# Performance work log

Measured on AMD Instinct MI355X. Metric: run time of the kernel, lower is better.

The kernel has to match this reference:

```python
import jax, jax.numpy as jnp
import numpy as np

B, T, D, H = 2, 2048, 2048, 16
HD = D // H  # head_dim = 128


def setup_inputs() -> dict:
    key = jax.random.key(0)
    ks = jax.random.split(key, 7)
    s = 1.0 / np.sqrt(D)
    return {
        "x": jax.random.normal(ks[0], (B, T, D), jnp.float32),
        "Wq": jax.random.normal(ks[1], (D, D), jnp.float32) * s,
        "Wk": jax.random.normal(ks[2], (D, D), jnp.float32) * s,
        "Wv": jax.random.normal(ks[3], (D, D), jnp.float32) * s,
        "Wo": jax.random.normal(ks[4], (D, D), jnp.float32) * s,
        "rope_cos": jax.random.uniform(ks[5], (T, HD), jnp.float32, -1.0, 1.0),
        "rope_sin": jax.random.uniform(ks[6], (T, HD), jnp.float32, -1.0, 1.0),
    }


def _rope(x, cos, sin):
    # x: [B,H,T,HD]; cos/sin: [T,HD] broadcast over batch/heads
    half = x.shape[-1] // 2
    lhs, rhs = x[..., :half], x[..., half:]
    rotated = jnp.concatenate((-rhs, lhs), axis=-1)
    return cos[None, None] * x + rotated * sin[None, None]


def reference(x, Wq, Wk, Wv, Wo, rope_cos, rope_sin):
    Bc, Tc, Dc = x.shape
    # torch nn.Linear: y = x @ W.T
    q = (x @ Wq.T).reshape(Bc, Tc, H, HD).transpose(0, 2, 1, 3)
    k = (x @ Wk.T).reshape(Bc, Tc, H, HD).transpose(0, 2, 1, 3)
    v = (x @ Wv.T).reshape(Bc, Tc, H, HD).transpose(0, 2, 1, 3)
    q = _rope(q, rope_cos[:Tc], rope_sin[:Tc])
    k = _rope(k, rope_cos[:Tc], rope_sin[:Tc])
    scores = jnp.einsum('bhqd,bhkd->bhqk', q, k) / jnp.sqrt(jnp.float32(HD))
    causal = jnp.triu(jnp.ones((Tc, Tc), bool), k=1)
    scores = jnp.where(causal[None, None], -jnp.inf, scores)
    attn = jax.nn.softmax(scores, axis=-1)
    ctx = jnp.einsum('bhqk,bhkd->bhqd', attn, v)
    ctx = ctx.transpose(0, 2, 1, 3).reshape(Bc, Tc, Dc)
    return ctx @ Wo.T
```

## Files before the change

kernel.cpp:

```cpp
#include <hip/hip_runtime.h>

typedef __attribute__((ext_vector_type(4))) float   f32x4;
typedef __attribute__((ext_vector_type(8))) __bf16  bf16x8;
typedef __attribute__((ext_vector_type(4))) __bf16  bf16x4;
typedef __attribute__((ext_vector_type(8))) unsigned short u16x8;

#define NH   16
#define HD   128
#define TSEQ 2048
#define DM   2048
#define MT   4096

__device__ __forceinline__ f32x4 mfma_bf16(bf16x8 a, bf16x8 b, f32x4 c) {
  return __builtin_amdgcn_mfma_f32_16x16x32_bf16(a, b, c, 0, 0, 0);
}

__device__ __forceinline__ void gl_lds16(const __bf16* g, __bf16* l) {
  __builtin_amdgcn_global_load_lds(
      (const __attribute__((address_space(1))) void*)g,
      (__attribute__((address_space(3))) void*)l, 16, 0, 0);
}

__global__ __launch_bounds__(256) void k_cvtw(
    const float* __restrict__ X,
    const float* __restrict__ W0, const float* __restrict__ W1,
    const float* __restrict__ W2, const float* __restrict__ W3,
    __bf16* __restrict__ DX,
    __bf16* __restrict__ D0, __bf16* __restrict__ D1,
    __bf16* __restrict__ D2, __bf16* __restrict__ D3) {
  int z = blockIdx.z;
  const float* s = (z == 0) ? W0 : (z == 1) ? W1 : (z == 2) ? W2
                   : (z == 3) ? W3 : X;
  __bf16*      d = (z == 0) ? D0 : (z == 1) ? D1 : (z == 2) ? D2
                   : (z == 3) ? D3 : DX;
  int n4 = (z == 4) ? (MT * DM / 4) : (DM * DM / 4);
  int i = blockIdx.x * 256 + threadIdx.x;
  int stride = gridDim.x * 256;
  for (; i < n4; i += stride) {
    f32x4 v = ((const f32x4*)s)[i];
    bf16x4 o;
    o[0] = (__bf16)v[0]; o[1] = (__bf16)v[1];
    o[2] = (__bf16)v[2]; o[3] = (__bf16)v[3];
    ((bf16x4*)d)[i] = o;
  }
}

template <int MODE>
__global__ __launch_bounds__(256) void k_gemm(const __bf16* __restrict__ A,
                                              const __bf16* __restrict__ Bm,
                                              __bf16* __restrict__ Dst,
                                              float* __restrict__ F) {
  __shared__ __bf16 As[128 * 32];
  __shared__ __bf16 Bs[128 * 32];

  const int bid = blockIdx.x;
  const int wg  = (bid & 7) * 64 + (bid >> 3);
  const int n0  = (wg & 15) * 128;
  const int m0  = (wg >> 4) * 128;

  const int tid  = threadIdx.x;
  const int lane = tid & 63, w = tid >> 6;
  const int g    = lane >> 4, li = lane & 15;
  const int wr   = w >> 1, wc = w & 1;
  const int srow = lane >> 2;
  const int sseg = lane & 3;

  const f32x4 zero = {0.f, 0.f, 0.f, 0.f};
  f32x4 acc[4][4];
#pragma unroll
  for (int i = 0; i < 4; i++)
#pragma unroll
    for (int j = 0; j < 4; j++) acc[i][j] = zero;

  for (int k0 = 0; k0 < DM; k0 += 32) {
#pragma unroll
    for (int c = 0; c < 2; c++) {
      const int ch = w * 2 + c;
      gl_lds16(&A[(size_t)(m0 + ch * 16 + srow) * DM + k0 + sseg * 8],
               &As[ch * 512]);
      gl_lds16(&Bm[(size_t)(n0 + ch * 16 + srow) * DM + k0 + sseg * 8],
               &Bs[ch * 512]);
    }
    __syncthreads();
    bf16x8 af[4], bfr[4];
#pragma unroll
    for (int i = 0; i < 4; i++)
      af[i] = *(const bf16x8*)&As[(wr * 64 + i * 16 + li) * 32 + g * 8];
#pragma unroll
    for (int i = 0; i < 4; i++)
      bfr[i] = *(const bf16x8*)&Bs[(wc * 64 + i * 16 + li) * 32 + g * 8];
#pragma unroll
    for (int mi = 0; mi < 4; mi++)
#pragma unroll
      for (int ni = 0; ni < 4; ni++)
        acc[mi][ni] = mfma_bf16(af[mi], bfr[ni], acc[mi][ni]);
    __syncthreads();
  }

#pragma unroll
  for (int mi = 0; mi < 4; mi++)
#pragma unroll
    for (int ni = 0; ni < 4; ni++) {
      int colb = n0 + wc * 64 + ni * 16 + li;
#pragma unroll
      for (int r = 0; r < 4; r++) {
        int rowb = m0 + wr * 64 + mi * 16 + g * 4 + r;
        float vv = acc[mi][ni][r];
        if (MODE == 0) {
          F[(size_t)rowb * DM + colb] = vv;
        } else {
          int h = colb >> 7, d = colb & 127;
          int b = rowb >> 11, t = rowb & 2047;
          Dst[(((size_t)(b * NH + h)) * TSEQ + t) * HD + d] = (__bf16)vv;
        }
      }
    }
}

__global__ __launch_bounds__(256) void k_rope(__bf16* __restrict__ q,
                                              __bf16* __restrict__ kk,
                                              const float* __restrict__ rc,
                                              const float* __restrict__ rs) {
  int gid    = blockIdx.x * 256 + threadIdx.x;
  int tensor = gid >> 20;
  int rem    = gid & ((1 << 20) - 1);
  int bh     = rem >> 15;
  int r2     = rem & 32767;
  int t      = r2 >> 4;
  int j      = r2 & 15;
  int d0     = j * 4;
  __bf16* base = (tensor ? kk : q) + ((size_t)bh * TSEQ + t) * HD;
  f32x4 ca = *(const f32x4*)&rc[t * HD + d0];
  f32x4 cb = *(const f32x4*)&rc[t * HD + d0 + 64];
  f32x4 sa = *(const f32x4*)&rs[t * HD + d0];
  f32x4 sb = *(const f32x4*)&rs[t * HD + d0 + 64];
  bf16x4 xa = *(bf16x4*)&base[d0];
  bf16x4 xb = *(bf16x4*)&base[d0 + 64];
  bf16x4 oa, ob;
#pragma unroll
  for (int u = 0; u < 4; u++) {
    float fa = (float)xa[u], fb = (float)xb[u];
    oa[u] = (__bf16)(ca[u] * fa - fb * sa[u]);
    ob[u] = (__bf16)(cb[u] * fb + fa * sb[u]);
  }
  *(bf16x4*)&base[d0]      = oa;
  *(bf16x4*)&base[d0 + 64] = ob;
}

__global__ __launch_bounds__(256) void k_trans(const __bf16* __restrict__ v,
                                               __bf16* __restrict__ vt) {
  __shared__ unsigned short tile[64][73];
  int bh = blockIdx.z;
  int t0 = blockIdx.x * 64, d0 = blockIdx.y * 64;
  int tid = threadIdx.x;
  int r = tid >> 2, s4 = tid & 3;
  const unsigned short* src =
      (const unsigned short*)v + ((size_t)bh * TSEQ + t0) * HD + d0;
  u16x8 a = *(const u16x8*)&src[(size_t)r * HD + s4 * 16];
  u16x8 b = *(const u16x8*)&src[(size_t)r * HD + s4 * 16 + 8];
#pragma unroll
  for (int u = 0; u < 8; u++) {
    tile[r][s4 * 16 + u]     = a[u];
    tile[r][s4 * 16 + 8 + u] = b[u];
  }
  __syncthreads();
  unsigned short* dst =
      (unsigned short*)vt + ((size_t)bh * HD + d0) * TSEQ + t0;
  u16x8 o1, o2;
#pragma unroll
  for (int u = 0; u < 8; u++) {
    o1[u] = tile[s4 * 16 + u][r];
    o2[u] = tile[s4 * 16 + 8 + u][r];
  }
  *(u16x8*)&dst[(size_t)r * TSEQ + s4 * 16]     = o1;
  *(u16x8*)&dst[(size_t)r * TSEQ + s4 * 16 + 8] = o2;
}

__global__ __launch_bounds__(256, 2) void k_attn(const __bf16* __restrict__ q,
                                                 const __bf16* __restrict__ k,
                                                 const __bf16* __restrict__ vt,
                                                 __bf16* __restrict__ ctx) {
  __shared__ __bf16 Ks[64 * 136];
  __shared__ __bf16 Vs[128 * 72];
  __shared__ __bf16 Ps[4][32 * 72];

  const int bid = blockIdx.x;
  const int wg  = (bid & 7) * 64 + (bid >> 3);
  const int bh  = wg >> 4;
  const int qt  = 15 - (wg & 15);
  const int q0  = qt * 128;

  const int tid  = threadIdx.x;
  const int lane = tid & 63, w = tid >> 6;
  const int g    = lane >> 4, li = lane & 15;
  const int qw   = q0 + w * 32;

  const __bf16* qb = q  + (size_t)bh * TSEQ * HD;
  const __bf16* kb = k  + (size_t)bh * TSEQ * HD;
  const __bf16* vb = vt + (size_t)bh * HD * TSEQ;

  const float CST = 0.08838834764831845f * 1.4426950408889634f;
  bf16x8 qf[2][4];
#pragma unroll
  for (int s = 0; s < 2; s++)
#pragma unroll
    for (int kc = 0; kc < 4; kc++) {
      bf16x8 t =
          *(const bf16x8*)&qb[(size_t)(qw + s * 16 + li) * HD + kc * 32 + g * 8];
      bf16x8 o;
#pragma unroll
      for (int e = 0; e < 8; e++) o[e] = (__bf16)((float)t[e] * CST);
      qf[s][kc] = o;
    }

  const f32x4 zero = {0.f, 0.f, 0.f, 0.f};
  f32x4 o[2][8];
#pragma unroll
  for (int s = 0; s < 2; s++)
#pragma unroll
    for (int dt = 0; dt < 8; dt++) o[s][dt] = zero;
  float mrow[2][4], lrow[2][4];
#pragma unroll
  for (int s = 0; s < 2; s++)
#pragma unroll
    for (int r = 0; r < 4; r++) { mrow[s][r] = -1e30f; lrow[s][r] = 0.f; }

  const int nkt = 2 * qt + 2;

  const int kR = tid >> 4, kS = tid & 15;
  const int vR = tid >> 3, vS = tid & 7;

  bf16x8 pk[4], pv[4];
#pragma unroll
  for (int i = 0; i < 4; i++) {
    pk[i] = *(const bf16x8*)&kb[(size_t)(kR + 16 * i) * HD + kS * 8];
    pv[i] = *(const bf16x8*)&vb[(size_t)(vR + 32 * i) * TSEQ + vS * 8];
  }

  for (int kt = 0; kt < nkt; kt++) {
    const int kv0 = kt * 64;
    __syncthreads();
#pragma unroll
    for (int i = 0; i < 4; i++)
      *(bf16x8*)&Ks[(kR + 16 * i) * 136 + kS * 8] = pk[i];
#pragma unroll
    for (int i = 0; i < 4; i++)
      *(bf16x8*)&Vs[(vR + 32 * i) * 72 + vS * 8] = pv[i];
    if (kt + 1 < nkt) {
      const int nv0 = kv0 + 64;
#pragma unroll
      for (int i = 0; i < 4; i++) {
        pk[i] = *(const bf16x8*)&kb[(size_t)(nv0 + kR + 16 * i) * HD + kS * 8];
        pv[i] = *(const bf16x8*)&vb[(size_t)(vR + 32 * i) * TSEQ + nv0 + vS * 8];
      }
    }
    __syncthreads();

    if (kv0 <= qw + 31) {
      f32x4 sc[2][4];
#pragma unroll
      for (int s = 0; s < 2; s++)
#pragma unroll
        for (int kvf = 0; kvf < 4; kvf++) sc[s][kvf] = zero;
#pragma unroll
      for (int kvf = 0; kvf < 4; kvf++)
#pragma unroll
        for (int kc = 0; kc < 4; kc++) {
          bf16x8 kf =
              *(const bf16x8*)&Ks[(kvf * 16 + li) * 136 + kc * 32 + g * 8];
          sc[0][kvf] = mfma_bf16(qf[0][kc], kf, sc[0][kvf]);
          sc[1][kvf] = mfma_bf16(qf[1][kc], kf, sc[1][kvf]);
        }
      if (kv0 + 63 > qw) {
#pragma unroll
        for (int s = 0; s < 2; s++)
#pragma unroll
          for (int kvf = 0; kvf < 4; kvf++) {
            int kg = kv0 + kvf * 16 + li;
#pragma unroll
            for (int r = 0; r < 4; r++) {
              int qg = qw + s * 16 + g * 4 + r;
              if (kg > qg) sc[s][kvf][r] = -1e30f;
            }
          }
      }
      float mnew[2][4];
      bool upd = false;
#pragma unroll
      for (int s = 0; s < 2; s++)
#pragma unroll
        for (int r = 0; r < 4; r++) {
          float a = fmaxf(fmaxf(sc[s][0][r], sc[s][1][r]),
                          fmaxf(sc[s][2][r], sc[s][3][r]));
          a = fmaxf(a, __shfl_xor(a, 1));
          a = fmaxf(a, __shfl_xor(a, 2));
          a = fmaxf(a, __shfl_xor(a, 4));
          a = fmaxf(a, __shfl_xor(a, 8));
          mnew[s][r] = fmaxf(mrow[s][r], a);
          upd = upd || (a > mrow[s][r]);
        }
      if (__any(upd)) {
#pragma unroll
        for (int s = 0; s < 2; s++)
#pragma unroll
          for (int r = 0; r < 4; r++) {
            float fac = __builtin_amdgcn_exp2f(mrow[s][r] - mnew[s][r]);
            mrow[s][r] = mnew[s][r];
            lrow[s][r] *= fac;
#pragma unroll
            for (int dt = 0; dt < 8; dt++) o[s][dt][r] *= fac;
          }
      }
#pragma unroll
      for (int s = 0; s < 2; s++)
#pragma unroll
        for (int kvf = 0; kvf < 4; kvf++) {
#pragma unroll
          for (int r = 0; r < 4; r++) {
            float p = __builtin_amdgcn_exp2f(sc[s][kvf][r] - mrow[s][r]);
            lrow[s][r] += p;
            Ps[w][(s * 16 + g * 4 + r) * 72 + kvf * 16 + li] = (__bf16)p;
          }
        }
      bf16x8 pa[2][2];
#pragma unroll
      for (int s = 0; s < 2; s++)
#pragma unroll
        for (int kvs = 0; kvs < 2; kvs++)
          pa[s][kvs] =
              *(const bf16x8*)&Ps[w][(s * 16 + li) * 72 + kvs * 32 + g * 8];
#pragma unroll
      for (int dt = 0; dt < 8; dt++) {
        bf16x8 v0 = *(const bf16x8*)&Vs[(dt * 16 + li) * 72 + g * 8];
        bf16x8 v1 = *(const bf16x8*)&Vs[(dt * 16 + li) * 72 + 32 + g * 8];
        o[0][dt] = mfma_bf16(pa[0][0], v0, o[0][dt]);
        o[0][dt] = mfma_bf16(pa[0][1], v1, o[0][dt]);
        o[1][dt] = mfma_bf16(pa[1][0], v0, o[1][dt]);
        o[1][dt] = mfma_bf16(pa[1][1], v1, o[1][dt]);
      }
    }
  }

  const int b = bh >> 4, h = bh & 15;
#pragma unroll
  for (int s = 0; s < 2; s++)
#pragma unroll
    for (int r = 0; r < 4; r++) {
      float l = lrow[s][r];
      l += __shfl_xor(l, 1);
      l += __shfl_xor(l, 2);
      l += __shfl_xor(l, 4);
      l += __shfl_xor(l, 8);
      float inv = 1.0f / l;
      size_t rowoff =
          ((size_t)(b * TSEQ + qw + s * 16 + g * 4 + r)) * DM + h * HD;
#pragma unroll
      for (int dt = 0; dt < 8; dt++)
        ctx[rowoff + dt * 16 + li] = (__bf16)(o[s][dt][r] * inv);
    }
}

extern "C" void kernel_launch(void* const* d_in, const int* in_sizes, int n_in,
                              void* d_out, int out_size, void* d_ws,
                              size_t ws_size, hipStream_t stream) {
  const float* x  = (const float*)d_in[0];
  const float* Wq = (const float*)d_in[1];
  const float* Wk = (const float*)d_in[2];
  const float* Wv = (const float*)d_in[3];
  const float* Wo = (const float*)d_in[4];
  const float* rc = (const float*)d_in[5];
  const float* rs = (const float*)d_in[6];
  float* out = (float*)d_out;

  __bf16* xb   = (__bf16*)d_ws;
  __bf16* wqb  = xb  + (size_t)MT * DM;
  __bf16* wkb  = wqb + (size_t)DM * DM;
  __bf16* wvb  = wkb + (size_t)DM * DM;
  __bf16* wob  = wvb + (size_t)DM * DM;
  __bf16* qbuf = wob + (size_t)DM * DM;
  __bf16* kbuf = qbuf + (size_t)MT * DM;
  __bf16* vbuf = kbuf + (size_t)MT * DM;
  __bf16* vtb  = vbuf + (size_t)MT * DM;
  __bf16* ctxb = vbuf;

  dim3 gw(1024, 1, 5);
  k_cvtw<<<gw, 256, 0, stream>>>(x, Wq, Wk, Wv, Wo, xb, wqb, wkb, wvb, wob);

  k_gemm<1><<<512, 256, 0, stream>>>(xb, wqb, qbuf, nullptr);
  k_gemm<1><<<512, 256, 0, stream>>>(xb, wkb, kbuf, nullptr);
  k_gemm<1><<<512, 256, 0, stream>>>(xb, wvb, vbuf, nullptr);

  k_rope<<<8192, 256, 0, stream>>>(qbuf, kbuf, rc, rs);

  dim3 gt(TSEQ / 64, HD / 64, 32);
  k_trans<<<gt, 256, 0, stream>>>(vbuf, vtb);

  k_attn<<<512, 256, 0, stream>>>(qbuf, kbuf, vtb, ctxb);

  k_gemm<0><<<512, 256, 0, stream>>>(ctxb, wob, nullptr, out);
}
```

Baseline: 456.9 us.

## Transpose QK^T MFMA so each lane owns one query row in softmax

Swaps the MFMA operand order for the score computation so the accumulator layout puts one query row per lane, with the KV positions spread over the four register elements. Row max and row sum then reduce mostly within a thread, needing 2 cross-lane shuffles instead of 4 per row, and per-thread softmax state shrinks from 8 to 2 scalars. P is written to LDS as packed 4-element vectors rather than scalar bf16 stores. In exchange, rescale factors and final inverses must be broadcast back to the O accumulator layout with extra __shfl calls, which adds cross-lane traffic on rescale steps.

Result: faster. 435.7 us (-4.6%).

```diff
diff --git a/kernel.cpp b/kernel.cpp
--- a/kernel.cpp
+++ b/kernel.cpp
@@ -219,11 +219,8 @@
   for (int s = 0; s < 2; s++)
 #pragma unroll
     for (int dt = 0; dt < 8; dt++) o[s][dt] = zero;
-  float mrow[2][4], lrow[2][4];
-#pragma unroll
-  for (int s = 0; s < 2; s++)
-#pragma unroll
-    for (int r = 0; r < 4; r++) { mrow[s][r] = -1e30f; lrow[s][r] = 0.f; }
+  float mrow[2] = {-1e30f, -1e30f};
+  float lrow[2] = {0.f, 0.f};
 
   const int nkt = 2 * qt + 2;
 
@@ -268,60 +265,68 @@
         for (int kc = 0; kc < 4; kc++) {
           bf16x8 kf =
               *(const bf16x8*)&Ks[(kvf * 16 + li) * 136 + kc * 32 + g * 8];
-          sc[0][kvf] = mfma_bf16(qf[0][kc], kf, sc[0][kvf]);
-          sc[1][kvf] = mfma_bf16(qf[1][kc], kf, sc[1][kvf]);
+          sc[0][kvf] = mfma_bf16(kf, qf[0][kc], sc[0][kvf]);
+          sc[1][kvf] = mfma_bf16(kf, qf[1][kc], sc[1][kvf]);
         }
       if (kv0 + 63 > qw) {
 #pragma unroll
-        for (int s = 0; s < 2; s++)
+        for (int s = 0; s < 2; s++) {
+          const int qg = qw + s * 16 + li;
 #pragma unroll
           for (int kvf = 0; kvf < 4; kvf++) {
-            int kg = kv0 + kvf * 16 + li;
 #pragma unroll
             for (int r = 0; r < 4; r++) {
-              int qg = qw + s * 16 + g * 4 + r;
+              int kg = kv0 + kvf * 16 + g * 4 + r;
               if (kg > qg) sc[s][kvf][r] = -1e30f;
             }
           }
-      }
-      float mnew[2][4];
+        }
+      }
+      float mnew[2];
       bool upd = false;
 #pragma unroll
-      for (int s = 0; s < 2; s++)
-#pragma unroll
-        for (int r = 0; r < 4; r++) {
-          float a = fmaxf(fmaxf(sc[s][0][r], sc[s][1][r]),
-                          fmaxf(sc[s][2][r], sc[s][3][r]));
-          a = fmaxf(a, __shfl_xor(a, 1));
-          a = fmaxf(a, __shfl_xor(a, 2));
-          a = fmaxf(a, __shfl_xor(a, 4));
-          a = fmaxf(a, __shfl_xor(a, 8));
-          mnew[s][r] = fmaxf(mrow[s][r], a);
-          upd = upd || (a > mrow[s][r]);
-        }
+      for (int s = 0; s < 2; s++) {
+        float a = fmaxf(fmaxf(sc[s][0][0], sc[s][0][1]),
+                        fmaxf(sc[s][0][2], sc[s][0][3]));
+#pragma unroll
+        for (int kvf = 1; kvf < 4; kvf++) {
+          float b0 = fmaxf(sc[s][kvf][0], sc[s][kvf][1]);
+          float b1 = fmaxf(sc[s][kvf][2], sc[s][kvf][3]);
+          a = fmaxf(a, fmaxf(b0, b1));
+        }
+        a = fmaxf(a, __shfl_xor(a, 16));
+        a = fmaxf(a, __shfl_xor(a, 32));
+        mnew[s] = fmaxf(mrow[s], a);
+        upd = upd || (a > mrow[s]);
+      }
       if (__any(upd)) {
 #pragma unroll
-        for (int s = 0; s < 2; s++)
+        for (int s = 0; s < 2; s++) {
+          float fc = __builtin_amdgcn_exp2f(mrow[s] - mnew[s]);
+          mrow[s] = mnew[s];
+          lrow[s] *= fc;
 #pragma unroll
           for (int r = 0; r < 4; r++) {
-            float fac = __builtin_amdgcn_exp2f(mrow[s][r] - mnew[s][r]);
-            mrow[s][r] = mnew[s][r];
-            lrow[s][r] *= fac;
-#pragma unroll
-            for (int dt = 0; dt < 8; dt++) o[s][dt][r] *= fac;
+            float fr = __shfl(fc, (lane & 48) | (g * 4 + r));
+#pragma unroll
+            for (int dt = 0; dt < 8; dt++) o[s][dt][r] *= fr;
           }
-      }
-#pragma unroll
-      for (int s = 0; s < 2; s++)
+        }
+      }
+#pragma unroll
+      for (int s = 0; s < 2; s++) {
 #pragma unroll
         for (int kvf = 0; kvf < 4; kvf++) {
+          bf16x4 pk4;
 #pragma unroll
           for (int r = 0; r < 4; r++) {
-            float p = __builtin_amdgcn_exp2f(sc[s][kvf][r] - mrow[s][r]);
-            lrow[s][r] += p;
-            Ps[w][(s * 16 + g * 4 + r) * 72 + kvf * 16 + li] = (__bf16)p;
+            float p = __builtin_amdgcn_exp2f(sc[s][kvf][r] - mrow[s]);
+            lrow[s] += p;
+            pk4[r] = (__bf16)p;
           }
-        }
+          *(bf16x4*)&Ps[w][(s * 16 + li) * 72 + kvf * 16 + g * 4] = pk4;
+        }
+      }
       bf16x8 pa[2][2];
 #pragma unroll
       for (int s = 0; s < 2; s++)
@@ -343,21 +348,21 @@
 
   const int b = bh >> 4, h = bh & 15;
 #pragma unroll
-  for (int s = 0; s < 2; s++)
+  for (int s = 0; s < 2; s++) {
+    float l = lrow[s];
+    l += __shfl_xor(l, 16);
+    l += __shfl_xor(l, 32);
+    float inv = 1.0f / l;
 #pragma unroll
     for (int r = 0; r < 4; r++) {
-      float l = lrow[s][r];
-      l += __shfl_xor(l, 1);
-      l += __shfl_xor(l, 2);
-      l += __shfl_xor(l, 4);
-      l += __shfl_xor(l, 8);
-      float inv = 1.0f / l;
+      float ir = __shfl(inv, (lane & 48) | (g * 4 + r));
       size_t rowoff =
           ((size_t)(b * TSEQ + qw + s * 16 + g * 4 + r)) * DM + h * HD;
 #pragma unroll
       for (int dt = 0; dt < 8; dt++)
-        ctx[rowoff + dt * 16 + li] = (__bf16)(o[s][dt][r] * inv);
-    }
+        ctx[rowoff + dt * 16 + li] = (__bf16)(o[s][dt][r] * ir);
+    }
+  }
 }
 
 extern "C" void kernel_launch(void* const* d_in, const int* in_sizes, int n_in,
```
